# Performance work log

Measured on AMD Instinct MI355X. Metric: run time of the kernel, lower is better.

The kernel has to match this reference:

```python
import jax, jax.numpy as jnp
import numpy as np

N_CLASSES = 1000
FEAT_DIM = 1024
PROJ_DIM = 256
BATCH = 32
NUM_SUPPORT = 8192


def setup_inputs() -> dict:
    key = jax.random.key(0)
    k1, k2, k3, k4 = jax.random.split(key, 4)
    x = jax.random.normal(k1, (BATCH, FEAT_DIM), dtype=jnp.float32)
    sx = jax.random.normal(k2, (NUM_SUPPORT, FEAT_DIM), dtype=jnp.float32)
    # xavier_uniform_ on (1, feat_dim, proj_dim): bound = sqrt(6/(feat+proj))
    bound = float(np.sqrt(6.0 / (FEAT_DIM + PROJ_DIM)))
    proj_weight = jax.random.uniform(k3, (FEAT_DIM, PROJ_DIM), dtype=jnp.float32,
                                     minval=-bound, maxval=bound)
    sy = jax.random.randint(k4, (NUM_SUPPORT,), 0, N_CLASSES, dtype=jnp.int64)
    return {"x": x, "sx": sx, "proj_weight": proj_weight, "sy": sy}


def reference(x, sx, proj_weight, sy):
    # One-hot support labels: (N, C)
    sy_oh = jax.nn.one_hot(sy, N_CLASSES, dtype=jnp.float32)
    # Low-rank projection (shared support set -> project once; identical math
    # to the original's per-batch bmm with a repeated weight).
    xq = x @ proj_weight            # (b, p)
    sxp = sx @ proj_weight          # (N, p)
    # Euclidean kernel: scores = -||xq_i - sxp_j||^2, shape (b, N)
    x_sq = jnp.sum(xq * xq, axis=-1, keepdims=True)       # (b, 1)
    s_sq = jnp.sum(sxp * sxp, axis=-1)[None, :]           # (1, N)
    scores = -(x_sq + s_sq - 2.0 * (xq @ sxp.T))          # (b, N)
    probs = jax.nn.softmax(scores, axis=-1)               # (b, N)
    out = probs @ sy_oh                                   # (b, C)
    return jnp.log(out + 1e-12)
```

## Files before the change

kernel.cpp:

```cpp
#include <hip/hip_runtime.h>
#include <math.h>

#define N_CLASSES 1000
#define FEAT_DIM 1024
#define PROJ_DIM 256
#define BATCH 32
#define NUM_SUPPORT 8192

#define PW_BLOCKS 16
#define PX_BLOCKS 256

typedef __attribute__((ext_vector_type(8))) _Float16 f16x8;
typedef __attribute__((ext_vector_type(2))) _Float16 f16x2;
typedef __attribute__((ext_vector_type(4))) float f32x4;

__global__ __launch_bounds__(256) void prelude_kernel(
    const float* __restrict__ W, const float* __restrict__ x,
    _Float16* __restrict__ W1, _Float16* __restrict__ xqh2) {
  __shared__ float part[256];
  __shared__ _Float16 Lw[256][66];
  const int bid = blockIdx.x;
  const int t = threadIdx.x;

  if (bid < PW_BLOCKS) {
    const int k0 = bid * 64;
#pragma unroll 8
    for (int kk = 0; kk < 64; kk++) {
      Lw[t][kk] = (_Float16)W[(size_t)(k0 + kk) * PROJ_DIM + t];
    }
    __syncthreads();
#pragma unroll
    for (int i = 0; i < 8; i++) {
      *(f16x8*)&W1[(size_t)t * FEAT_DIM + k0 + i * 8] = *(f16x8*)&Lw[t][i * 8];
    }
  } else {
    const int pxb = bid - PW_BLOCKS;
    const int b = pxb >> 3, cc = pxb & 7;
    const int col = t & 31, ks = t >> 5;
    const int gc = cc * 32 + col;
    const int k0 = ks * 128;
    float s = 0.f;
#pragma unroll 8
    for (int k = 0; k < 128; k++) {
      s = fmaf(x[(size_t)b * FEAT_DIM + k0 + k],
               W[(size_t)(k0 + k) * PROJ_DIM + gc], s);
    }
    part[t] = s;
    __syncthreads();
    if (t < 32) {
      float acc = 0.f;
#pragma unroll
      for (int i = 0; i < 8; i++) acc += part[i * 32 + t];
      xqh2[(size_t)b * PROJ_DIM + cc * 32 + t] = (_Float16)(2.0f * acc);
    }
  }
}

__global__ __launch_bounds__(256) void gemm_score_kernel(
    const float* __restrict__ sx, const _Float16* __restrict__ W1,
    const _Float16* __restrict__ xqh2, float* __restrict__ scP) {
  __shared__ _Float16 At[32 * 64];
  __shared__ _Float16 Bt[64 * 64];
  __shared__ _Float16 Sx[32 * 72];
  __shared__ _Float16 Xl[32 * 64];

  const int tid = threadIdx.x;
  const int w = tid >> 6;
  const int lane = tid & 63;
  const int xcd = blockIdx.x & 7;
  const int idx = blockIdx.x >> 3;
  const int bm = (xcd * 32 + (idx & 31)) * 32;
  const int ntile = idx >> 5;
  const int bn = ntile * 64;
  const int wm = w & 1, wn = w >> 1;
  const int m16 = lane & 15, quad = lane >> 4;
  const int lrow8 = lane >> 3;
  const int gB = (lane & 7) ^ lrow8;

  {
    const int r = tid >> 3, c = tid & 7;
    *(f16x8*)&Xl[r * 64 + c * 8] =
        *(const f16x8*)&xqh2[(size_t)r * PROJ_DIM + bn + c * 8];
  }

  const int arow = tid >> 3;
  const int ac = tid & 7;
  const float* __restrict__ abase =
      sx + (size_t)(bm + arow) * FEAT_DIM + ac * 8;
  _Float16* __restrict__ ad = &At[arow * 64 + (ac ^ (arow & 7)) * 8];

  f32x4 acc[2];
#pragma unroll
  for (int nt = 0; nt < 2; nt++) acc[nt] = (f32x4){0.f, 0.f, 0.f, 0.f};

  for (int kb = 0; kb < FEAT_DIM; kb += 64) {
    {
      const float4* gp = (const float4*)(abase + kb);
      const float4 v0 = gp[0], v1 = gp[1];
      f16x8 h0 = {(_Float16)v0.x, (_Float16)v0.y, (_Float16)v0.z,
                  (_Float16)v0.w, (_Float16)v1.x, (_Float16)v1.y,
                  (_Float16)v1.z, (_Float16)v1.w};
      *(f16x8*)ad = h0;
    }
#pragma unroll
    for (int i = 0; i < 2; i++) {
      const int nrow = w * 16 + i * 8 + lrow8;
      const _Float16* gp = W1 + (size_t)(bn + nrow) * FEAT_DIM + kb + gB * 8;
      __builtin_amdgcn_global_load_lds(
          (const __attribute__((address_space(1))) void*)gp,
          (__attribute__((address_space(3))) void*)(Bt + (w * 16 + i * 8) * 64),
          16, 0, 0);
    }
    __syncthreads();

#pragma unroll
    for (int s = 0; s < 2; s++) {
      const int slot = (s * 4 + quad) ^ (m16 & 7);
      f16x8 af, bf[2];
      {
        const int row = wm * 16 + m16;
        af = *(f16x8*)&At[row * 64 + slot * 8];
      }
#pragma unroll
      for (int nt = 0; nt < 2; nt++) {
        const int nrow = wn * 32 + nt * 16 + m16;
        bf[nt] = *(f16x8*)&Bt[nrow * 64 + slot * 8];
      }
#pragma unroll
      for (int nt = 0; nt < 2; nt++)
        acc[nt] = __builtin_amdgcn_mfma_f32_16x16x32_f16(af, bf[nt], acc[nt],
                                                         0, 0, 0);
    }
    __syncthreads();
  }

#pragma unroll
  for (int nt = 0; nt < 2; nt++)
#pragma unroll
    for (int r = 0; r < 4; r++) {
      const int jl = wm * 16 + quad * 4 + r;
      const int nl = wn * 32 + nt * 16 + m16;
      Sx[jl * 72 + nl] = (_Float16)acc[nt][r];
    }
  __syncthreads();

  const int j = tid & 31;
  const int bg = tid >> 5;
  float dotb[4] = {0.f, 0.f, 0.f, 0.f};
  float rsq = 0.f;
#pragma unroll
  for (int c = 0; c < 8; c++) {
    const f16x8 hv = *(const f16x8*)&Sx[j * 72 + c * 8];
    const f16x2* hp = (const f16x2*)&hv;
#pragma unroll
    for (int i = 0; i < 4; i++)
      rsq = __builtin_amdgcn_fdot2(hp[i], hp[i], rsq, false);
#pragma unroll
    for (int b4 = 0; b4 < 4; b4++) {
      const f16x8 xv = *(const f16x8*)&Xl[(bg * 4 + b4) * 64 + c * 8];
      const f16x2* xp = (const f16x2*)&xv;
#pragma unroll
      for (int i = 0; i < 4; i++)
        dotb[b4] = __builtin_amdgcn_fdot2(hp[i], xp[i], dotb[b4], false);
    }
  }
  float* __restrict__ outP = scP + (size_t)ntile * BATCH * NUM_SUPPORT;
#pragma unroll
  for (int b4 = 0; b4 < 4; b4++) {
    outP[(size_t)(bg * 4 + b4) * NUM_SUPPORT + bm + j] = dotb[b4] - rsq;
  }
}

__global__ __launch_bounds__(1024) void finish_kernel(
    const float* __restrict__ scP, const int* __restrict__ sy,
    float* __restrict__ out) {
  __shared__ float cls[N_CLASSES];
  __shared__ float redm[16];
  __shared__ float reds[16];

  const int b = blockIdx.x;
  const int t = threadIdx.x;
  const int lane = t & 63, wave = t >> 6;
  const size_t P = (size_t)BATCH * NUM_SUPPORT;
  const float* __restrict__ row0 = scP + (size_t)b * NUM_SUPPORT;

  float v[8];
  float m = -1e30f;
#pragma unroll
  for (int jj = 0; jj < 8; jj++) {
    const size_t o = (size_t)jj * 1024 + t;
    v[jj] = (row0[o] + row0[P + o]) + (row0[2 * P + o] + row0[3 * P + o]);
    m = fmaxf(m, v[jj]);
  }
#pragma unroll
  for (int o = 1; o < 64; o <<= 1) m = fmaxf(m, __shfl_xor(m, o, 64));
  if (lane == 0) redm[wave] = m;
  if (t < N_CLASSES) cls[t] = 0.0f;
  __syncthreads();
  float gm = redm[0];
#pragma unroll
  for (int i = 1; i < 16; i++) gm = fmaxf(gm, redm[i]);

  float lsum = 0.0f;
#pragma unroll
  for (int jj = 0; jj < 8; jj++) {
    const float e = expf(v[jj] - gm);
    lsum += e;
    atomicAdd(&cls[sy[jj * 1024 + t]], e);
  }
#pragma unroll
  for (int o = 1; o < 64; o <<= 1) lsum += __shfl_xor(lsum, o, 64);
  if (lane == 0) reds[wave] = lsum;
  __syncthreads();
  float total = 0.f;
#pragma unroll
  for (int i = 0; i < 16; i++) total += reds[i];
  const float inv = 1.0f / total;
  if (t < N_CLASSES) {
    out[(size_t)b * N_CLASSES + t] = logf(cls[t] * inv + 1e-12f);
  }
}

extern "C" void kernel_launch(void* const* d_in, const int* in_sizes, int n_in,
                              void* d_out, int out_size, void* d_ws,
                              size_t ws_size, hipStream_t stream) {
  const float* x = (const float*)d_in[0];
  const float* sx = (const float*)d_in[1];
  const float* W = (const float*)d_in[2];
  const int* sy = (const int*)d_in[3];
  float* out = (float*)d_out;

  char* p = (char*)d_ws;
  float* scP = (float*)p;         p += (size_t)4 * BATCH * NUM_SUPPORT * 4;
  _Float16* W1 = (_Float16*)p;    p += (size_t)PROJ_DIM * FEAT_DIM * 2;
  _Float16* xqh2 = (_Float16*)p;

  prelude_kernel<<<dim3(PW_BLOCKS + PX_BLOCKS), dim3(256), 0, stream>>>(
      W, x, W1, xqh2);
  gemm_score_kernel<<<dim3(1024), dim3(256), 0, stream>>>(sx, W1, xqh2, scP);
  finish_kernel<<<dim3(BATCH), dim3(1024), 0, stream>>>(scP, sy, out);
}
```

Before: 111.2 us.

## Widen GEMM N-tile to 128, use 32x32 MFMA with register-prefetched double buffering

The projection GEMM now computes 128 projected columns per block instead of 64, halving the grid and the number of partial score slices the finish kernel must sum. The main loop switches to 32x32x16 MFMA, keeps W fragments in registers, prefetches the next sx and W slice one step ahead, and double-buffers the A tile in LDS. The score epilogue now uses MFMA for the dot products against the query, with a shuffle reduction for the squared norms. Each block redundantly reads the whole sx tile twice rather than four times, at the cost of more registers per thread and lower occupancy.

Result: slower. 116.9 us (+5.0%).

```diff
diff --git a/kernel.cpp b/kernel.cpp
--- a/kernel.cpp
+++ b/kernel.cpp
@@ -11,8 +11,8 @@
 #define PX_BLOCKS 256
 
 typedef __attribute__((ext_vector_type(8))) _Float16 f16x8;
-typedef __attribute__((ext_vector_type(2))) _Float16 f16x2;
 typedef __attribute__((ext_vector_type(4))) float f32x4;
+typedef __attribute__((ext_vector_type(16))) float f32x16;
 
 __global__ __launch_bounds__(256) void prelude_kernel(
     const float* __restrict__ W, const float* __restrict__ x,
@@ -59,115 +59,133 @@
 __global__ __launch_bounds__(256) void gemm_score_kernel(
     const float* __restrict__ sx, const _Float16* __restrict__ W1,
     const _Float16* __restrict__ xqh2, float* __restrict__ scP) {
-  __shared__ _Float16 At[32 * 64];
-  __shared__ _Float16 Bt[64 * 64];
-  __shared__ _Float16 Sx[32 * 72];
-  __shared__ _Float16 Xl[32 * 64];
+  __shared__ _Float16 At[2][32 * 64];
+  __shared__ _Float16 Sx[32 * 128];
+  __shared__ _Float16 Xl[32 * 128];
+  __shared__ float Rp[4][32];
+  __shared__ float Rt[32];
 
   const int tid = threadIdx.x;
   const int w = tid >> 6;
   const int lane = tid & 63;
+  const int l31 = lane & 31;
+  const int hi = lane >> 5;
+
   const int xcd = blockIdx.x & 7;
   const int idx = blockIdx.x >> 3;
   const int bm = (xcd * 32 + (idx & 31)) * 32;
   const int ntile = idx >> 5;
-  const int bn = ntile * 64;
-  const int wm = w & 1, wn = w >> 1;
-  const int m16 = lane & 15, quad = lane >> 4;
-  const int lrow8 = lane >> 3;
-  const int gB = (lane & 7) ^ lrow8;
-
-  {
-    const int r = tid >> 3, c = tid & 7;
-    *(f16x8*)&Xl[r * 64 + c * 8] =
-        *(const f16x8*)&xqh2[(size_t)r * PROJ_DIM + bn + c * 8];
+  const int bn = ntile * 128;
+
+  {
+    const int r = tid >> 3;
+    const int c0 = tid & 7;
+#pragma unroll
+    for (int cc = 0; cc < 2; cc++) {
+      const int c = c0 + cc * 8;
+      const int sw = (c & 8) | ((c & 7) ^ (r & 7));
+      *(f16x8*)&Xl[r * 128 + sw * 8] =
+          *(const f16x8*)&xqh2[(size_t)r * PROJ_DIM + bn + c * 8];
+    }
   }
 
   const int arow = tid >> 3;
   const int ac = tid & 7;
   const float* __restrict__ abase =
       sx + (size_t)(bm + arow) * FEAT_DIM + ac * 8;
-  _Float16* __restrict__ ad = &At[arow * 64 + (ac ^ (arow & 7)) * 8];
-
-  f32x4 acc[2];
-#pragma unroll
-  for (int nt = 0; nt < 2; nt++) acc[nt] = (f32x4){0.f, 0.f, 0.f, 0.f};
-
-  for (int kb = 0; kb < FEAT_DIM; kb += 64) {
-    {
-      const float4* gp = (const float4*)(abase + kb);
-      const float4 v0 = gp[0], v1 = gp[1];
-      f16x8 h0 = {(_Float16)v0.x, (_Float16)v0.y, (_Float16)v0.z,
-                  (_Float16)v0.w, (_Float16)v1.x, (_Float16)v1.y,
-                  (_Float16)v1.z, (_Float16)v1.w};
-      *(f16x8*)ad = h0;
-    }
-#pragma unroll
-    for (int i = 0; i < 2; i++) {
-      const int nrow = w * 16 + i * 8 + lrow8;
-      const _Float16* gp = W1 + (size_t)(bn + nrow) * FEAT_DIM + kb + gB * 8;
-      __builtin_amdgcn_global_load_lds(
-          (const __attribute__((address_space(1))) void*)gp,
-          (__attribute__((address_space(3))) void*)(Bt + (w * 16 + i * 8) * 64),
-          16, 0, 0);
+  const int asw = (ac ^ (arow & 7)) * 8;
+
+  const _Float16* __restrict__ bbase =
+      W1 + (size_t)(bn + w * 32 + l31) * FEAT_DIM + hi * 8;
+
+  f32x16 acc;
+#pragma unroll
+  for (int i = 0; i < 16; ++i) acc[i] = 0.f;
+
+  {
+    const float4* gp = (const float4*)abase;
+    const float4 v0 = gp[0], v1 = gp[1];
+    f16x8 h = {(_Float16)v0.x, (_Float16)v0.y, (_Float16)v0.z, (_Float16)v0.w,
+               (_Float16)v1.x, (_Float16)v1.y, (_Float16)v1.z, (_Float16)v1.w};
+    *(f16x8*)&At[0][arow * 64 + asw] = h;
+  }
+  f16x8 bcur[4];
+#pragma unroll
+  for (int ks = 0; ks < 4; ks++) bcur[ks] = *(const f16x8*)&bbase[ks * 16];
+  __syncthreads();
+
+#pragma unroll
+  for (int t = 0; t < 16; ++t) {
+    const int cur = t & 1;
+    const int kb = t * 64;
+    float4 a0, a1;
+    f16x8 bnx[4];
+    if (t < 15) {
+      const float4* gp = (const float4*)(abase + kb + 64);
+      a0 = gp[0];
+      a1 = gp[1];
+#pragma unroll
+      for (int ks = 0; ks < 4; ks++)
+        bnx[ks] = *(const f16x8*)&bbase[kb + 64 + ks * 16];
+    }
+#pragma unroll
+    for (int ks = 0; ks < 4; ks++) {
+      const int c = ks * 2 + hi;
+      const int sw = (c ^ (l31 & 7)) * 8;
+      const f16x8 af = *(const f16x8*)&At[cur][l31 * 64 + sw];
+      acc = __builtin_amdgcn_mfma_f32_32x32x16_f16(af, bcur[ks], acc, 0, 0, 0);
+    }
+    if (t < 15) {
+      f16x8 h = {(_Float16)a0.x, (_Float16)a0.y, (_Float16)a0.z,
+                 (_Float16)a0.w, (_Float16)a1.x, (_Float16)a1.y,
+                 (_Float16)a1.z, (_Float16)a1.w};
+      *(f16x8*)&At[cur ^ 1][arow * 64 + asw] = h;
+#pragma unroll
+      for (int ks = 0; ks < 4; ks++) bcur[ks] = bnx[ks];
     }
     __syncthreads();
-
-#pragma unroll
-    for (int s = 0; s < 2; s++) {
-      const int slot = (s * 4 + quad) ^ (m16 & 7);
-      f16x8 af, bf[2];
-      {
-        const int row = wm * 16 + m16;
-        af = *(f16x8*)&At[row * 64 + slot * 8];
-      }
-#pragma unroll
-      for (int nt = 0; nt < 2; nt++) {
-        const int nrow = wn * 32 + nt * 16 + m16;
-        bf[nt] = *(f16x8*)&Bt[nrow * 64 + slot * 8];
-      }
-#pragma unroll
-      for (int nt = 0; nt < 2; nt++)
-        acc[nt] = __builtin_amdgcn_mfma_f32_16x16x32_f16(af, bf[nt], acc[nt],
-                                                         0, 0, 0);
-    }
-    __syncthreads();
-  }
-
-#pragma unroll
-  for (int nt = 0; nt < 2; nt++)
-#pragma unroll
-    for (int r = 0; r < 4; r++) {
-      const int jl = wm * 16 + quad * 4 + r;
-      const int nl = wn * 32 + nt * 16 + m16;
-      Sx[jl * 72 + nl] = (_Float16)acc[nt][r];
-    }
-  __syncthreads();
-
-  const int j = tid & 31;
-  const int bg = tid >> 5;
-  float dotb[4] = {0.f, 0.f, 0.f, 0.f};
-  float rsq = 0.f;
-#pragma unroll
-  for (int c = 0; c < 8; c++) {
-    const f16x8 hv = *(const f16x8*)&Sx[j * 72 + c * 8];
-    const f16x2* hp = (const f16x2*)&hv;
-#pragma unroll
-    for (int i = 0; i < 4; i++)
-      rsq = __builtin_amdgcn_fdot2(hp[i], hp[i], rsq, false);
-#pragma unroll
-    for (int b4 = 0; b4 < 4; b4++) {
-      const f16x8 xv = *(const f16x8*)&Xl[(bg * 4 + b4) * 64 + c * 8];
-      const f16x2* xp = (const f16x2*)&xv;
-#pragma unroll
-      for (int i = 0; i < 4; i++)
-        dotb[b4] = __builtin_amdgcn_fdot2(hp[i], xp[i], dotb[b4], false);
-    }
-  }
-  float* __restrict__ outP = scP + (size_t)ntile * BATCH * NUM_SUPPORT;
-#pragma unroll
-  for (int b4 = 0; b4 < 4; b4++) {
-    outP[(size_t)(bg * 4 + b4) * NUM_SUPPORT + bm + j] = dotb[b4] - rsq;
+  }
+
+#pragma unroll
+  for (int r = 0; r < 16; ++r) {
+    float p = acc[r] * acc[r];
+#pragma unroll
+    for (int m = 1; m <= 16; m <<= 1) p += __shfl_xor(p, m, 64);
+    if (l31 == 0) Rp[w][(r & 3) + 8 * (r >> 2) + 4 * hi] = p;
+  }
+  {
+    const int n = w * 32 + l31;
+    const int cb = n >> 3, nin = n & 7;
+#pragma unroll
+    for (int r = 0; r < 16; ++r) {
+      const int j = (r & 3) + 8 * (r >> 2) + 4 * hi;
+      const int sw = (cb & 8) | ((cb & 7) ^ (j & 7));
+      Sx[j * 128 + sw * 8 + nin] = (_Float16)acc[r];
+    }
+  }
+  __syncthreads();
+  if (tid < 32) Rt[tid] = Rp[0][tid] + Rp[1][tid] + Rp[2][tid] + Rp[3][tid];
+  __syncthreads();
+
+  f32x16 sc;
+#pragma unroll
+  for (int i = 0; i < 16; ++i) sc[i] = 0.f;
+#pragma unroll
+  for (int ks = 0; ks < 8; ++ks) {
+    const int c = ks * 2 + hi;
+    const int sw = ((c & 8) | ((c & 7) ^ (l31 & 7))) * 8;
+    const f16x8 af = *(const f16x8*)&Sx[l31 * 128 + sw];
+    const f16x8 bf = *(const f16x8*)&Xl[l31 * 128 + sw];
+    sc = __builtin_amdgcn_mfma_f32_32x32x16_f16(af, bf, sc, 0, 0, 0);
+  }
+  {
+    const int b = l31;
+    const int j0 = 8 * w + 4 * hi;
+    f32x4 v;
+#pragma unroll
+    for (int r = 0; r < 4; ++r) v[r] = sc[w * 4 + r] - Rt[j0 + r];
+    float* __restrict__ outP = scP + (size_t)ntile * BATCH * NUM_SUPPORT;
+    *(f32x4*)&outP[(size_t)b * NUM_SUPPORT + bm + j0] = v;
   }
 }
 
@@ -189,7 +207,7 @@
 #pragma unroll
   for (int jj = 0; jj < 8; jj++) {
     const size_t o = (size_t)jj * 1024 + t;
-    v[jj] = (row0[o] + row0[P + o]) + (row0[2 * P + o] + row0[3 * P + o]);
+    v[jj] = row0[o] + row0[P + o];
     m = fmaxf(m, v[jj]);
   }
 #pragma unroll
@@ -231,12 +249,12 @@
   float* out = (float*)d_out;
 
   char* p = (char*)d_ws;
-  float* scP = (float*)p;         p += (size_t)4 * BATCH * NUM_SUPPORT * 4;
+  float* scP = (float*)p;         p += (size_t)2 * BATCH * NUM_SUPPORT * 4;
   _Float16* W1 = (_Float16*)p;    p += (size_t)PROJ_DIM * FEAT_DIM * 2;
   _Float16* xqh2 = (_Float16*)p;
 
   prelude_kernel<<<dim3(PW_BLOCKS + PX_BLOCKS), dim3(256), 0, stream>>>(
       W, x, W1, xqh2);
-  gemm_score_kernel<<<dim3(1024), dim3(256), 0, stream>>>(sx, W1, xqh2, scP);
+  gemm_score_kernel<<<dim3(512), dim3(256), 0, stream>>>(sx, W1, xqh2, scP);
   finish_kernel<<<dim3(BATCH), dim3(1024), 0, stream>>>(scP, sy, out);
 }
```

## Double-buffer LDS tiles in score GEMM to overlap loads with MFMA

Applied to the files above, without the earlier changes.

Doubles the A and B shared-memory tiles and prefetches the next K-slice (the fp32 sx registers plus the async W1 global_load_lds) before running the MFMAs on the current slice. The converted A tile is written into the alternate buffer after compute, so each iteration needs one barrier instead of two. This aims to hide global-memory latency behind compute, at the cost of twice the LDS and more live registers, which may lower occupancy.

Measured after the change: 113.7 us. +2.2%, slower.

```diff
diff --git a/kernel.cpp b/kernel.cpp
--- a/kernel.cpp
+++ b/kernel.cpp
@@ -59,8 +59,8 @@
 __global__ __launch_bounds__(256) void gemm_score_kernel(
     const float* __restrict__ sx, const _Float16* __restrict__ W1,
     const _Float16* __restrict__ xqh2, float* __restrict__ scP) {
-  __shared__ _Float16 At[32 * 64];
-  __shared__ _Float16 Bt[64 * 64];
+  __shared__ _Float16 At[2][32 * 64];
+  __shared__ _Float16 Bt[2][64 * 64];
   __shared__ _Float16 Sx[32 * 72];
   __shared__ _Float16 Xl[32 * 64];
 
@@ -87,31 +87,53 @@
   const int ac = tid & 7;
   const float* __restrict__ abase =
       sx + (size_t)(bm + arow) * FEAT_DIM + ac * 8;
-  _Float16* __restrict__ ad = &At[arow * 64 + (ac ^ (arow & 7)) * 8];
+  const int asw = (ac ^ (arow & 7)) * 8;
 
   f32x4 acc[2];
 #pragma unroll
   for (int nt = 0; nt < 2; nt++) acc[nt] = (f32x4){0.f, 0.f, 0.f, 0.f};
 
-  for (int kb = 0; kb < FEAT_DIM; kb += 64) {
-    {
-      const float4* gp = (const float4*)(abase + kb);
-      const float4 v0 = gp[0], v1 = gp[1];
-      f16x8 h0 = {(_Float16)v0.x, (_Float16)v0.y, (_Float16)v0.z,
-                  (_Float16)v0.w, (_Float16)v1.x, (_Float16)v1.y,
-                  (_Float16)v1.z, (_Float16)v1.w};
-      *(f16x8*)ad = h0;
-    }
-#pragma unroll
-    for (int i = 0; i < 2; i++) {
-      const int nrow = w * 16 + i * 8 + lrow8;
-      const _Float16* gp = W1 + (size_t)(bn + nrow) * FEAT_DIM + kb + gB * 8;
-      __builtin_amdgcn_global_load_lds(
-          (const __attribute__((address_space(1))) void*)gp,
-          (__attribute__((address_space(3))) void*)(Bt + (w * 16 + i * 8) * 64),
-          16, 0, 0);
-    }
-    __syncthreads();
+  {
+    const float4* gp = (const float4*)abase;
+    const float4 v0 = gp[0], v1 = gp[1];
+    f16x8 h0 = {(_Float16)v0.x, (_Float16)v0.y, (_Float16)v0.z, (_Float16)v0.w,
+                (_Float16)v1.x, (_Float16)v1.y, (_Float16)v1.z, (_Float16)v1.w};
+    *(f16x8*)&At[0][arow * 64 + asw] = h0;
+  }
+#pragma unroll
+  for (int i = 0; i < 2; i++) {
+    const int nrow = w * 16 + i * 8 + lrow8;
+    const _Float16* gp = W1 + (size_t)(bn + nrow) * FEAT_DIM + gB * 8;
+    __builtin_amdgcn_global_load_lds(
+        (const __attribute__((address_space(1))) void*)gp,
+        (__attribute__((address_space(3))) void*)(Bt[0] +
+                                                  (w * 16 + i * 8) * 64),
+        16, 0, 0);
+  }
+  __syncthreads();
+
+  for (int t = 0; t < 16; ++t) {
+    const int cur = t & 1;
+    const int nb = cur ^ 1;
+    const int kb = t * 64;
+
+    float4 a0, a1;
+    if (t < 15) {
+      const float4* gp = (const float4*)(abase + kb + 64);
+      a0 = gp[0];
+      a1 = gp[1];
+#pragma unroll
+      for (int i = 0; i < 2; i++) {
+        const int nrow = w * 16 + i * 8 + lrow8;
+        const _Float16* gp2 =
+            W1 + (size_t)(bn + nrow) * FEAT_DIM + kb + 64 + gB * 8;
+        __builtin_amdgcn_global_load_lds(
+            (const __attribute__((address_space(1))) void*)gp2,
+            (__attribute__((address_space(3))) void*)(Bt[nb] +
+                                                      (w * 16 + i * 8) * 64),
+            16, 0, 0);
+      }
+    }
 
 #pragma unroll
     for (int s = 0; s < 2; s++) {
@@ -119,17 +141,24 @@
       f16x8 af, bf[2];
       {
         const int row = wm * 16 + m16;
-        af = *(f16x8*)&At[row * 64 + slot * 8];
+        af = *(f16x8*)&At[cur][row * 64 + slot * 8];
       }
 #pragma unroll
       for (int nt = 0; nt < 2; nt++) {
         const int nrow = wn * 32 + nt * 16 + m16;
-        bf[nt] = *(f16x8*)&Bt[nrow * 64 + slot * 8];
+        bf[nt] = *(f16x8*)&Bt[cur][nrow * 64 + slot * 8];
       }
 #pragma unroll
       for (int nt = 0; nt < 2; nt++)
         acc[nt] = __builtin_amdgcn_mfma_f32_16x16x32_f16(af, bf[nt], acc[nt],
                                                          0, 0, 0);
+    }
+
+    if (t < 15) {
+      f16x8 h = {(_Float16)a0.x, (_Float16)a0.y, (_Float16)a0.z,
+                 (_Float16)a0.w, (_Float16)a1.x, (_Float16)a1.y,
+                 (_Float16)a1.z, (_Float16)a1.w};
+      *(f16x8*)&At[nb][arow * 64 + asw] = h;
     }
     __syncthreads();
   }
```
